# Kernel tuning notes

Measured on AMD Instinct MI355X. Metric: run time of the kernel, lower is better.

The kernel has to match this reference:

```python
import jax, jax.numpy as jnp
import numpy as np

N_NODES = 10000
N_EDGES = 640000
DIM = 128


def setup_inputs() -> dict:
    key = jax.random.key(0)
    ks = jax.random.split(key, 10)
    s = 1.0 / np.sqrt(DIM)
    return {
        "x": jax.random.normal(ks[0], (N_NODES, DIM), dtype=jnp.float32),
        "edge_index": jax.random.randint(ks[1], (2, N_EDGES), 0, N_NODES, dtype=jnp.int64),
        "fc_w": jax.random.normal(ks[2], (DIM, DIM), dtype=jnp.float32) * s,
        "fc_b": jax.random.normal(ks[3], (DIM,), dtype=jnp.float32) * s,
        "f_lw": jax.random.normal(ks[4], (DIM, DIM), dtype=jnp.float32) * s,
        "f_lb": jax.random.normal(ks[5], (DIM,), dtype=jnp.float32) * s,
        "f_rw": jax.random.normal(ks[6], (DIM, DIM), dtype=jnp.float32) * s,
        "n_lw": jax.random.normal(ks[7], (DIM, DIM), dtype=jnp.float32) * s,
        "n_lb": jax.random.normal(ks[8], (DIM,), dtype=jnp.float32) * s,
        "n_rw": jax.random.normal(ks[9], (DIM, DIM), dtype=jnp.float32) * s,
    }


def _sage_conv(h, src, dst, lw, lb, rw, n_nodes):
    # mean aggregation of source-node features at target nodes
    msg = h[src]                                                   # [E, D]
    summed = jax.ops.segment_sum(msg, dst, num_segments=n_nodes)   # [N, D]
    cnt = jax.ops.segment_sum(jnp.ones_like(dst, dtype=h.dtype), dst, num_segments=n_nodes)
    agg = summed / jnp.maximum(cnt, 1.0)[:, None]
    # PyG SAGEConv: lin_l(agg) + lin_r(x); lin_l has bias, lin_r does not
    return agg @ lw.T + lb + h @ rw.T


def reference(x, edge_index, fc_w, fc_b, f_lw, f_lb, f_rw, n_lw, n_lb, n_rw):
    n_nodes = x.shape[0]
    src, dst = edge_index[0], edge_index[1]
    inp = x @ fc_w.T + fc_b                                        # fc residual branch
    h = jax.nn.relu(_sage_conv(x, src, dst, f_lw, f_lb, f_rw, n_nodes))
    # dropout(p=0.3) is identity in eval mode
    h = _sage_conv(h, src, dst, n_lw, n_lb, n_rw, n_nodes)
    return jax.nn.relu(h + inp)
```

## Files before the change

### kernel.cpp

```cpp
#include <hip/hip_runtime.h>
#include <hip/hip_fp8.h>

#define NN 10000
#define NE 640000
#define DIM 128
#define NB 157
#define REGCAP 4608
#define MT1 157
#define EPB 4096
#define G_FILL 157
#define NODECAP 128

typedef __attribute__((ext_vector_type(8))) short bf16x8;
typedef __attribute__((ext_vector_type(4))) float f32x4;

__device__ __forceinline__ unsigned short f2bf(float f) {
    unsigned u = __float_as_uint(f);
    u += 0x7FFFu + ((u >> 16) & 1u);
    return (unsigned short)(u >> 16);
}
__device__ __forceinline__ float bf2f(unsigned short h) {
    return __uint_as_float(((unsigned)h) << 16);
}
__device__ __forceinline__ unsigned char f2f8(float f) {
    __hip_fp8_e4m3 t(f);
    return (unsigned char)t.__x;
}
__device__ __forceinline__ float f82f(unsigned char u) {
    __hip_fp8_e4m3 t;
    t.__x = (__hip_fp8_storage_t)u;
    return (float)t;
}

__global__ __launch_bounds__(256) void prep_k(
        const float* __restrict__ w0, const float* __restrict__ w1,
        const float* __restrict__ w2, const float* __restrict__ w3,
        const float* __restrict__ w4,
        unsigned short* __restrict__ wb, int* __restrict__ gcur) {
    int t = blockIdx.x * 256 + threadIdx.x;
    if (t < 256) gcur[t] = 0;
    int plane = t >> 14;
    int i = t & 16383;
    const float* wp = (plane == 0) ? w0 : (plane == 1) ? w1 :
                      (plane == 2) ? w2 : (plane == 3) ? w3 : w4;
    wb[t] = f2bf(wp[i]);
}

__global__ __launch_bounds__(256) void mega1_k(
        const float* __restrict__ A,
        const unsigned short* __restrict__ wb,
        unsigned char* __restrict__ xl8,
        float* __restrict__ xr, float* __restrict__ xc,
        const int* __restrict__ src, const int* __restrict__ dst,
        int* __restrict__ gcur, unsigned* __restrict__ region) {
    int b = blockIdx.x;
    int tid = threadIdx.x;
    if (b < G_FILL) {
        __shared__ int start[NB + 1];
        __shared__ int cur[NB];
        __shared__ int gbase[NB];
        __shared__ unsigned sorted[EPB];
        if (tid < NB + 1) start[tid] = 0;
        __syncthreads();
        int base = b * EPB;
        int nE = min(EPB, NE - base);
        unsigned pk[4][4];
        int kb[4][4];
        bool cv[4];
#pragma unroll
        for (int c = 0; c < 4; ++c) {
            int e = base + c * 1024 + tid * 4;
            cv[c] = (e < NE);
            if (cv[c]) {
                int4 s = *(const int4*)(src + e);
                int4 d = *(const int4*)(dst + e);
                pk[c][0] = ((unsigned)d.x << 16) | (unsigned)s.x;
                pk[c][1] = ((unsigned)d.y << 16) | (unsigned)s.y;
                pk[c][2] = ((unsigned)d.z << 16) | (unsigned)s.z;
                pk[c][3] = ((unsigned)d.w << 16) | (unsigned)s.w;
                kb[c][0] = d.x >> 6; kb[c][1] = d.y >> 6;
                kb[c][2] = d.z >> 6; kb[c][3] = d.w >> 6;
            }
        }
#pragma unroll
        for (int c = 0; c < 4; ++c)
            if (cv[c])
#pragma unroll
                for (int j = 0; j < 4; ++j) atomicAdd(&start[kb[c][j] + 1], 1);
        __syncthreads();
        for (int off = 1; off < NB + 1; off <<= 1) {
            int v = 0;
            if (tid <= NB && tid >= off) v = start[tid - off];
            __syncthreads();
            if (tid <= NB && tid >= off) start[tid] += v;
            __syncthreads();
        }
        if (tid < NB) cur[tid] = start[tid];
        __syncthreads();
#pragma unroll
        for (int c = 0; c < 4; ++c)
            if (cv[c])
#pragma unroll
                for (int j = 0; j < 4; ++j) {
                    int q = atomicAdd(&cur[kb[c][j]], 1);
                    sorted[q] = pk[c][j];
                }
        __syncthreads();
        if (tid < NB) {
            int len = start[tid + 1] - start[tid];
            gbase[tid] = (len > 0) ? atomicAdd(&gcur[tid], len) : 0;
        }
        __syncthreads();
        for (int i = tid; i < nE; i += 256) {
            unsigned e = sorted[i];
            int bb = (int)(e >> 16) >> 6;
            int rel = gbase[bb] + (i - start[bb]);
            if (rel < REGCAP) region[(size_t)bb * REGCAP + rel] = e;
        }
        return;
    }
    int gb = b - G_FILL;
    int plane = gb / MT1;
    int mt = gb % MT1;
    const unsigned short* W = wb + (size_t)plane * (DIM * DIM);
    int lane = tid & 63;
    int wv = tid >> 6;
    int mr = lane & 15, q = lane >> 4;
    int m0 = mt * 64 + wv * 16;
    int mc = min(m0 + mr, NN - 1);

    bf16x8 afr[4];
#pragma unroll
    for (int kc = 0; kc < 4; ++kc) {
        const float* ap = A + (size_t)mc * DIM + kc * 32 + q * 8;
        float4 v0 = *(const float4*)ap;
        float4 v1 = *(const float4*)(ap + 4);
        bf16x8 f;
        f[0] = (short)f2bf(v0.x); f[1] = (short)f2bf(v0.y);
        f[2] = (short)f2bf(v0.z); f[3] = (short)f2bf(v0.w);
        f[4] = (short)f2bf(v1.x); f[5] = (short)f2bf(v1.y);
        f[6] = (short)f2bf(v1.z); f[7] = (short)f2bf(v1.w);
        afr[kc] = f;
    }
    f32x4 acc[8];
#pragma unroll
    for (int nt = 0; nt < 8; ++nt) acc[nt] = (f32x4){0.f, 0.f, 0.f, 0.f};
#pragma unroll
    for (int nt = 0; nt < 8; ++nt) {
        const unsigned short* wp = W + (size_t)(nt * 16 + mr) * DIM;
#pragma unroll
        for (int kc = 0; kc < 4; ++kc) {
            bf16x8 wfr = *(const bf16x8*)(const void*)(wp + kc * 32 + q * 8);
            acc[nt] = __builtin_amdgcn_mfma_f32_16x16x32_bf16(afr[kc], wfr, acc[nt], 0, 0, 0);
        }
    }
#pragma unroll
    for (int r = 0; r < 4; ++r) {
        int ms = m0 + q * 4 + r;
        if (ms >= NN) continue;
        if (plane == 0) {
#pragma unroll
            for (int nt = 0; nt < 8; ++nt)
                xl8[(size_t)ms * DIM + nt * 16 + mr] = f2f8(acc[nt][r]);
        } else {
            float* o = (plane == 1) ? xr : xc;
#pragma unroll
            for (int nt = 0; nt < 8; ++nt)
                o[(size_t)ms * DIM + nt * 16 + mr] = acc[nt][r];
        }
    }
}

template<int MODE>
__global__ __launch_bounds__(256) void agg_k(
        const unsigned char* __restrict__ g8,
        const float* __restrict__ xr, const float* __restrict__ b0v,
        const int* __restrict__ gcur, const unsigned* __restrict__ region,
        unsigned short* __restrict__ outb, unsigned char* __restrict__ out8) {
    int blk = blockIdx.x;
    int b = blk >> 2, sub = blk & 3;
    int n0 = b * 64 + sub * 16;
    int tid = threadIdx.x;
    __shared__ unsigned short list[16][NODECAP];
    __shared__ int cnt[16];
    if (tid < 16) cnt[tid] = 0;
    __syncthreads();
    int R = min(gcur[b], REGCAP);
    const unsigned* reg = region + (size_t)b * REGCAP;
    for (int i = tid; i < R; i += 256) {
        unsigned e = reg[i];
        int nl = (int)(e >> 16) - n0;
        if ((unsigned)nl < 16u) {
            int slot = atomicAdd(&cnt[nl], 1);
            if (slot < NODECAP) list[nl][slot] = (unsigned short)(e & 0xFFFFu);
        }
    }
    __syncthreads();

    int g = tid >> 4, d8 = tid & 15;
    int node = n0 + g;
    if (node >= NN) return;
    int trueDeg = cnt[g];
    int deg = min(trueDeg, NODECAP);
    float a[8];
#pragma unroll
    for (int j = 0; j < 8; ++j) a[j] = 0.f;
    union U { uint2 v; unsigned char c[8]; };
    int r = 0;
    for (; r + 8 <= deg; r += 8) {
        U u[8];
#pragma unroll
        for (int t = 0; t < 8; ++t) {
            int i0 = list[g][r + t];
            u[t].v = *(const uint2*)(const void*)(g8 + (size_t)i0 * DIM + d8 * 8);
        }
#pragma unroll
        for (int t = 0; t < 8; ++t)
#pragma unroll
            for (int j = 0; j < 8; ++j) a[j] += f82f(u[t].c[j]);
    }
    for (; r < deg; ++r) {
        int i0 = list[g][r];
        U u0;
        u0.v = *(const uint2*)(const void*)(g8 + (size_t)i0 * DIM + d8 * 8);
#pragma unroll
        for (int j = 0; j < 8; ++j) a[j] += f82f(u0.c[j]);
    }
    float inv = 1.f / fmaxf((float)trueDeg, 1.f);
    union B { int4 v; unsigned short us[8]; } o;
    if (MODE == 0) {
        const float* xp = xr + (size_t)node * DIM + d8 * 8;
        float4 r0 = *(const float4*)xp;
        float4 r1 = *(const float4*)(xp + 4);
        const float* bp = b0v + d8 * 8;
        float4 c0 = *(const float4*)bp;
        float4 c1 = *(const float4*)(bp + 4);
        float rv[8] = {r0.x, r0.y, r0.z, r0.w, r1.x, r1.y, r1.z, r1.w};
        float bv[8] = {c0.x, c0.y, c0.z, c0.w, c1.x, c1.y, c1.z, c1.w};
        U o8;
#pragma unroll
        for (int j = 0; j < 8; ++j) {
            float v = fmaxf(a[j] * inv + rv[j] + bv[j], 0.f);
            o.us[j] = f2bf(v);
            o8.c[j] = f2f8(v);
        }
        *(int4*)(void*)(outb + (size_t)node * DIM + d8 * 8) = o.v;
        *(uint2*)(void*)(out8 + (size_t)node * DIM + d8 * 8) = o8.v;
    } else {
#pragma unroll
        for (int j = 0; j < 8; ++j) o.us[j] = f2bf(a[j] * inv);
        *(int4*)(void*)(outb + (size_t)node * DIM + d8 * 8) = o.v;
    }
}

__global__ __launch_bounds__(128) void mega2_k(
        const unsigned short* __restrict__ m1b,
        const unsigned short* __restrict__ h1b,
        const unsigned short* __restrict__ wb,
        const float* __restrict__ xc,
        const float* __restrict__ nlb, const float* __restrict__ fcb,
        float* __restrict__ out) {
    const unsigned short* W0 = wb + (size_t)3 * DIM * DIM;
    const unsigned short* W1 = wb + (size_t)4 * DIM * DIM;
    int lane = threadIdx.x & 63;
    int wv = threadIdx.x >> 6;
    int mr = lane & 15, q = lane >> 4;
    int m0 = (int)blockIdx.x * 32 + wv * 16;
    int mc = min(m0 + mr, NN - 1);

    bf16x8 a0[4], a1[4];
#pragma unroll
    for (int kc = 0; kc < 4; ++kc) {
        a0[kc] = *(const bf16x8*)(const void*)(m1b + (size_t)mc * DIM + kc * 32 + q * 8);
        a1[kc] = *(const bf16x8*)(const void*)(h1b + (size_t)mc * DIM + kc * 32 + q * 8);
    }
    f32x4 acc[8];
#pragma unroll
    for (int nt = 0; nt < 8; ++nt) acc[nt] = (f32x4){0.f, 0.f, 0.f, 0.f};
#pragma unroll
    for (int nt = 0; nt < 8; ++nt) {
        const unsigned short* w0p = W0 + (size_t)(nt * 16 + mr) * DIM;
        const unsigned short* w1p = W1 + (size_t)(nt * 16 + mr) * DIM;
#pragma unroll
        for (int kc = 0; kc < 4; ++kc) {
            bf16x8 wf0 = *(const bf16x8*)(const void*)(w0p + kc * 32 + q * 8);
            acc[nt] = __builtin_amdgcn_mfma_f32_16x16x32_bf16(a0[kc], wf0, acc[nt], 0, 0, 0);
            bf16x8 wf1 = *(const bf16x8*)(const void*)(w1p + kc * 32 + q * 8);
            acc[nt] = __builtin_amdgcn_mfma_f32_16x16x32_bf16(a1[kc], wf1, acc[nt], 0, 0, 0);
        }
    }
    float bias[8];
#pragma unroll
    for (int nt = 0; nt < 8; ++nt) {
        int col = nt * 16 + mr;
        bias[nt] = nlb[col] + fcb[col];
    }
#pragma unroll
    for (int r = 0; r < 4; ++r) {
        int ms = m0 + q * 4 + r;
        if (ms >= NN) continue;
#pragma unroll
        for (int nt = 0; nt < 8; ++nt) {
            int col = nt * 16 + mr;
            float v = acc[nt][r] + xc[(size_t)ms * DIM + col] + bias[nt];
            out[(size_t)ms * DIM + col] = fmaxf(v, 0.f);
        }
    }
}

extern "C" void kernel_launch(void* const* d_in, const int* in_sizes, int n_in,
                              void* d_out, int out_size, void* d_ws, size_t ws_size,
                              hipStream_t stream) {
    const float* x    = (const float*)d_in[0];
    const int*   edge = (const int*)d_in[1];
    const float* fc_w = (const float*)d_in[2];
    const float* fc_b = (const float*)d_in[3];
    const float* f_lw = (const float*)d_in[4];
    const float* f_lb = (const float*)d_in[5];
    const float* f_rw = (const float*)d_in[6];
    const float* n_lw = (const float*)d_in[7];
    const float* n_lb = (const float*)d_in[8];
    const float* n_rw = (const float*)d_in[9];
    float* out = (float*)d_out;

    const int* src = edge;
    const int* dst = edge + NE;

    char* p = (char*)d_ws;
    float* xr = (float*)p;                     p += (size_t)NN * DIM * sizeof(float);
    float* xc = (float*)p;                     p += (size_t)NN * DIM * sizeof(float);
    unsigned short* h1b = (unsigned short*)p;  p += (size_t)NN * DIM * sizeof(unsigned short);
    unsigned short* m1b = (unsigned short*)p;  p += (size_t)NN * DIM * sizeof(unsigned short);
    unsigned short* wb  = (unsigned short*)p;  p += (size_t)5 * DIM * DIM * sizeof(unsigned short);
    unsigned char* xl8  = (unsigned char*)p;   p += (size_t)NN * DIM;
    unsigned char* h18  = (unsigned char*)p;   p += (size_t)NN * DIM;
    int* gcur = (int*)p;                       p += (size_t)256 * sizeof(int);
    unsigned* region = (unsigned*)p;

    prep_k<<<(5 * DIM * DIM) / 256, 256, 0, stream>>>(f_lw, f_rw, fc_w, n_lw, n_rw, wb, gcur);
    mega1_k<<<G_FILL + 3 * MT1, 256, 0, stream>>>(
        x, wb, xl8, xr, xc, src, dst, gcur, region);
    agg_k<0><<<4 * NB, 256, 0, stream>>>(xl8, xr, f_lb, gcur, region, h1b, h18);
    agg_k<1><<<4 * NB, 256, 0, stream>>>(h18, nullptr, nullptr, gcur, region, m1b, nullptr);
    mega2_k<<<2 * MT1, 128, 0, stream>>>(m1b, h1b, wb, xc, n_lb, fc_b, out);
}
```

Baseline: 145.1 us.

## Overlap second-layer root GEMM with aggregation and widen gather unroll

Moves the h1 @ n_rw GEMM out of the final kernel and into extra blocks of the second aggregation kernel, so it runs concurrently with the edge gather. The result is written to the xr buffer, which is dead by then, and the final kernel adds it back. The gather loop also gains a 16-deep unrolled stage to keep more loads in flight. The trade-off is an extra fp32 N×D write and read round trip, plus more register pressure in the gather.

After: 145.2 us. Within noise of the previous version (+0.0%).

```diff
diff --git a/kernel.cpp b/kernel.cpp
--- a/kernel.cpp
+++ b/kernel.cpp
@@ -9,6 +9,7 @@
 #define MT1 157
 #define EPB 4096
 #define G_FILL 157
+#define G_AGG 628
 #define NODECAP 128
 
 typedef __attribute__((ext_vector_type(8))) short bf16x8;
@@ -171,8 +172,46 @@
     }
 }
 
-template<int MODE>
-__global__ __launch_bounds__(256) void agg_k(
+__device__ __forceinline__ void agg_gather(
+        const unsigned char* __restrict__ g8,
+        const unsigned short list[16][NODECAP], int g, int d8, int deg,
+        float a[8]) {
+    union U { uint2 v; unsigned char c[8]; };
+    int r = 0;
+    for (; r + 16 <= deg; r += 16) {
+        U u[16];
+#pragma unroll
+        for (int t = 0; t < 16; ++t) {
+            int i0 = list[g][r + t];
+            u[t].v = *(const uint2*)(const void*)(g8 + (size_t)i0 * DIM + d8 * 8);
+        }
+#pragma unroll
+        for (int t = 0; t < 16; ++t)
+#pragma unroll
+            for (int j = 0; j < 8; ++j) a[j] += f82f(u[t].c[j]);
+    }
+    for (; r + 8 <= deg; r += 8) {
+        U u[8];
+#pragma unroll
+        for (int t = 0; t < 8; ++t) {
+            int i0 = list[g][r + t];
+            u[t].v = *(const uint2*)(const void*)(g8 + (size_t)i0 * DIM + d8 * 8);
+        }
+#pragma unroll
+        for (int t = 0; t < 8; ++t)
+#pragma unroll
+            for (int j = 0; j < 8; ++j) a[j] += f82f(u[t].c[j]);
+    }
+    for (; r < deg; ++r) {
+        int i0 = list[g][r];
+        U u0;
+        u0.v = *(const uint2*)(const void*)(g8 + (size_t)i0 * DIM + d8 * 8);
+#pragma unroll
+        for (int j = 0; j < 8; ++j) a[j] += f82f(u0.c[j]);
+    }
+}
+
+__global__ __launch_bounds__(256) void agg1_k(
         const unsigned char* __restrict__ g8,
         const float* __restrict__ xr, const float* __restrict__ b0v,
         const int* __restrict__ gcur, const unsigned* __restrict__ region,
@@ -201,92 +240,133 @@
     int node = n0 + g;
     if (node >= NN) return;
     int trueDeg = cnt[g];
-    int deg = min(trueDeg, NODECAP);
     float a[8];
 #pragma unroll
     for (int j = 0; j < 8; ++j) a[j] = 0.f;
-    union U { uint2 v; unsigned char c[8]; };
-    int r = 0;
-    for (; r + 8 <= deg; r += 8) {
-        U u[8];
-#pragma unroll
-        for (int t = 0; t < 8; ++t) {
-            int i0 = list[g][r + t];
-            u[t].v = *(const uint2*)(const void*)(g8 + (size_t)i0 * DIM + d8 * 8);
-        }
-#pragma unroll
-        for (int t = 0; t < 8; ++t)
-#pragma unroll
-            for (int j = 0; j < 8; ++j) a[j] += f82f(u[t].c[j]);
-    }
-    for (; r < deg; ++r) {
-        int i0 = list[g][r];
-        U u0;
-        u0.v = *(const uint2*)(const void*)(g8 + (size_t)i0 * DIM + d8 * 8);
-#pragma unroll
-        for (int j = 0; j < 8; ++j) a[j] += f82f(u0.c[j]);
-    }
+    agg_gather(g8, list, g, d8, min(trueDeg, NODECAP), a);
     float inv = 1.f / fmaxf((float)trueDeg, 1.f);
+    const float* xp = xr + (size_t)node * DIM + d8 * 8;
+    float4 r0 = *(const float4*)xp;
+    float4 r1 = *(const float4*)(xp + 4);
+    const float* bp = b0v + d8 * 8;
+    float4 c0 = *(const float4*)bp;
+    float4 c1 = *(const float4*)(bp + 4);
+    float rv[8] = {r0.x, r0.y, r0.z, r0.w, r1.x, r1.y, r1.z, r1.w};
+    float bv[8] = {c0.x, c0.y, c0.z, c0.w, c1.x, c1.y, c1.z, c1.w};
     union B { int4 v; unsigned short us[8]; } o;
-    if (MODE == 0) {
-        const float* xp = xr + (size_t)node * DIM + d8 * 8;
-        float4 r0 = *(const float4*)xp;
-        float4 r1 = *(const float4*)(xp + 4);
-        const float* bp = b0v + d8 * 8;
-        float4 c0 = *(const float4*)bp;
-        float4 c1 = *(const float4*)(bp + 4);
-        float rv[8] = {r0.x, r0.y, r0.z, r0.w, r1.x, r1.y, r1.z, r1.w};
-        float bv[8] = {c0.x, c0.y, c0.z, c0.w, c1.x, c1.y, c1.z, c1.w};
-        U o8;
-#pragma unroll
-        for (int j = 0; j < 8; ++j) {
-            float v = fmaxf(a[j] * inv + rv[j] + bv[j], 0.f);
-            o.us[j] = f2bf(v);
-            o8.c[j] = f2f8(v);
-        }
-        *(int4*)(void*)(outb + (size_t)node * DIM + d8 * 8) = o.v;
-        *(uint2*)(void*)(out8 + (size_t)node * DIM + d8 * 8) = o8.v;
-    } else {
+    union U8 { uint2 v; unsigned char c[8]; } o8;
+#pragma unroll
+    for (int j = 0; j < 8; ++j) {
+        float v = fmaxf(a[j] * inv + rv[j] + bv[j], 0.f);
+        o.us[j] = f2bf(v);
+        o8.c[j] = f2f8(v);
+    }
+    *(int4*)(void*)(outb + (size_t)node * DIM + d8 * 8) = o.v;
+    *(uint2*)(void*)(out8 + (size_t)node * DIM + d8 * 8) = o8.v;
+}
+
+__global__ __launch_bounds__(256) void agg2g_k(
+        const unsigned char* __restrict__ h18,
+        const unsigned short* __restrict__ h1b,
+        const unsigned short* __restrict__ wb,
+        const int* __restrict__ gcur, const unsigned* __restrict__ region,
+        unsigned short* __restrict__ m1b, float* __restrict__ ur) {
+    int blk = blockIdx.x;
+    int tid = threadIdx.x;
+    if (blk < G_AGG) {
+        int b = blk >> 2, sub = blk & 3;
+        int n0 = b * 64 + sub * 16;
+        __shared__ unsigned short list[16][NODECAP];
+        __shared__ int cnt[16];
+        if (tid < 16) cnt[tid] = 0;
+        __syncthreads();
+        int R = min(gcur[b], REGCAP);
+        const unsigned* reg = region + (size_t)b * REGCAP;
+        for (int i = tid; i < R; i += 256) {
+            unsigned e = reg[i];
+            int nl = (int)(e >> 16) - n0;
+            if ((unsigned)nl < 16u) {
+                int slot = atomicAdd(&cnt[nl], 1);
+                if (slot < NODECAP) list[nl][slot] = (unsigned short)(e & 0xFFFFu);
+            }
+        }
+        __syncthreads();
+        int g = tid >> 4, d8 = tid & 15;
+        int node = n0 + g;
+        if (node >= NN) return;
+        int trueDeg = cnt[g];
+        float a[8];
+#pragma unroll
+        for (int j = 0; j < 8; ++j) a[j] = 0.f;
+        agg_gather(h18, list, g, d8, min(trueDeg, NODECAP), a);
+        float inv = 1.f / fmaxf((float)trueDeg, 1.f);
+        union B { int4 v; unsigned short us[8]; } o;
 #pragma unroll
         for (int j = 0; j < 8; ++j) o.us[j] = f2bf(a[j] * inv);
-        *(int4*)(void*)(outb + (size_t)node * DIM + d8 * 8) = o.v;
+        *(int4*)(void*)(m1b + (size_t)node * DIM + d8 * 8) = o.v;
+        return;
+    }
+    int gb = blk - G_AGG;
+    const unsigned short* W = wb + (size_t)4 * DIM * DIM;
+    int lane = tid & 63;
+    int wv = tid >> 6;
+    int mr = lane & 15, q = lane >> 4;
+    int m0 = gb * 64 + wv * 16;
+    int mc = min(m0 + mr, NN - 1);
+
+    bf16x8 afr[4];
+#pragma unroll
+    for (int kc = 0; kc < 4; ++kc)
+        afr[kc] = *(const bf16x8*)(const void*)(h1b + (size_t)mc * DIM + kc * 32 + q * 8);
+    f32x4 acc[8];
+#pragma unroll
+    for (int nt = 0; nt < 8; ++nt) acc[nt] = (f32x4){0.f, 0.f, 0.f, 0.f};
+#pragma unroll
+    for (int nt = 0; nt < 8; ++nt) {
+        const unsigned short* wp = W + (size_t)(nt * 16 + mr) * DIM;
+#pragma unroll
+        for (int kc = 0; kc < 4; ++kc) {
+            bf16x8 wfr = *(const bf16x8*)(const void*)(wp + kc * 32 + q * 8);
+            acc[nt] = __builtin_amdgcn_mfma_f32_16x16x32_bf16(afr[kc], wfr, acc[nt], 0, 0, 0);
+        }
+    }
+#pragma unroll
+    for (int r = 0; r < 4; ++r) {
+        int ms = m0 + q * 4 + r;
+        if (ms >= NN) continue;
+#pragma unroll
+        for (int nt = 0; nt < 8; ++nt)
+            ur[(size_t)ms * DIM + nt * 16 + mr] = acc[nt][r];
     }
 }
 
 __global__ __launch_bounds__(128) void mega2_k(
         const unsigned short* __restrict__ m1b,
-        const unsigned short* __restrict__ h1b,
         const unsigned short* __restrict__ wb,
-        const float* __restrict__ xc,
+        const float* __restrict__ ur, const float* __restrict__ xc,
         const float* __restrict__ nlb, const float* __restrict__ fcb,
         float* __restrict__ out) {
     const unsigned short* W0 = wb + (size_t)3 * DIM * DIM;
-    const unsigned short* W1 = wb + (size_t)4 * DIM * DIM;
     int lane = threadIdx.x & 63;
     int wv = threadIdx.x >> 6;
     int mr = lane & 15, q = lane >> 4;
     int m0 = (int)blockIdx.x * 32 + wv * 16;
     int mc = min(m0 + mr, NN - 1);
 
-    bf16x8 a0[4], a1[4];
-#pragma unroll
-    for (int kc = 0; kc < 4; ++kc) {
+    bf16x8 a0[4];
+#pragma unroll
+    for (int kc = 0; kc < 4; ++kc)
         a0[kc] = *(const bf16x8*)(const void*)(m1b + (size_t)mc * DIM + kc * 32 + q * 8);
-        a1[kc] = *(const bf16x8*)(const void*)(h1b + (size_t)mc * DIM + kc * 32 + q * 8);
-    }
     f32x4 acc[8];
 #pragma unroll
     for (int nt = 0; nt < 8; ++nt) acc[nt] = (f32x4){0.f, 0.f, 0.f, 0.f};
 #pragma unroll
     for (int nt = 0; nt < 8; ++nt) {
         const unsigned short* w0p = W0 + (size_t)(nt * 16 + mr) * DIM;
-        const unsigned short* w1p = W1 + (size_t)(nt * 16 + mr) * DIM;
 #pragma unroll
         for (int kc = 0; kc < 4; ++kc) {
             bf16x8 wf0 = *(const bf16x8*)(const void*)(w0p + kc * 32 + q * 8);
             acc[nt] = __builtin_amdgcn_mfma_f32_16x16x32_bf16(a0[kc], wf0, acc[nt], 0, 0, 0);
-            bf16x8 wf1 = *(const bf16x8*)(const void*)(w1p + kc * 32 + q * 8);
-            acc[nt] = __builtin_amdgcn_mfma_f32_16x16x32_bf16(a1[kc], wf1, acc[nt], 0, 0, 0);
         }
     }
     float bias[8];
@@ -302,7 +382,8 @@
 #pragma unroll
         for (int nt = 0; nt < 8; ++nt) {
             int col = nt * 16 + mr;
-            float v = acc[nt][r] + xc[(size_t)ms * DIM + col] + bias[nt];
+            float v = acc[nt][r] + ur[(size_t)ms * DIM + col]
+                    + xc[(size_t)ms * DIM + col] + bias[nt];
             out[(size_t)ms * DIM + col] = fmaxf(v, 0.f);
         }
     }
@@ -340,7 +421,7 @@
     prep_k<<<(5 * DIM * DIM) / 256, 256, 0, stream>>>(f_lw, f_rw, fc_w, n_lw, n_rw, wb, gcur);
     mega1_k<<<G_FILL + 3 * MT1, 256, 0, stream>>>(
         x, wb, xl8, xr, xc, src, dst, gcur, region);
-    agg_k<0><<<4 * NB, 256, 0, stream>>>(xl8, xr, f_lb, gcur, region, h1b, h18);
-    agg_k<1><<<4 * NB, 256, 0, stream>>>(h18, nullptr, nullptr, gcur, region, m1b, nullptr);
-    mega2_k<<<2 * MT1, 128, 0, stream>>>(m1b, h1b, wb, xc, n_lb, fc_b, out);
-}
+    agg1_k<<<G_AGG, 256, 0, stream>>>(xl8, xr, f_lb, gcur, region, h1b, h18);
+    agg2g_k<<<G_AGG + MT1, 256, 0, stream>>>(h18, h1b, wb, gcur, region, m1b, xr);
+    mega2_k<<<2 * MT1, 128, 0, stream>>>(m1b, wb, xr, xc, n_lb, fc_b, out);
+}
```
